# Performance work log

Measured on AMD Instinct MI355X. Metric: run time of the kernel, lower is better.

The kernel has to match this reference:

```python
import jax, jax.numpy as jnp
import numpy as np

TEMPERATURE = 8.0  # sqrt(d_k) with d_k = 64
NEG_INF = -jnp.inf


def setup_inputs() -> dict:
    key = jax.random.key(0)
    kq, kk, kv = jax.random.split(key, 3)
    b, n, d = 16, 2048, 64
    q = jax.random.normal(kq, (b, n, d), dtype=jnp.float32)
    k = jax.random.normal(kk, (b, n, d), dtype=jnp.float32)
    v = jax.random.normal(kv, (b, n, d), dtype=jnp.float32)
    # causal mask: True where attention is disallowed (strict upper triangle)
    mask = jnp.broadcast_to(jnp.triu(jnp.ones((n, n), dtype=bool), k=1), (b, n, n))
    return {"q": q, "k": k, "v": v, "mask": mask}


def reference(q, k, v, mask):
    # attn = q @ k^T / temperature   [b, n, n]
    attn = jnp.einsum('bqd,bkd->bqk', q, k) / TEMPERATURE
    attn = jnp.where(mask, NEG_INF, attn)
    attn = jax.nn.softmax(attn, axis=2)
    # output = attn @ v   [b, n, d]
    output = jnp.einsum('bqk,bkd->bqd', attn, v)
    return (output, attn)
```

## Files before the change

### kernel.cpp

```cpp
#include <hip/hip_runtime.h>


constexpr int B = 16;
constexpr int N = 2048;
constexpr int D = 64;
constexpr float INV_TEMP = 0.125f;

typedef __attribute__((ext_vector_type(8))) short bf16x8;
typedef __attribute__((ext_vector_type(4))) float f32x4;

__device__ __forceinline__ short f2bf(float f) {
    __bf16 h = (__bf16)f;
    return __builtin_bit_cast(short, h);
}

__global__ __launch_bounds__(256) void sdpa_mfma(
    const float* __restrict__ q,
    const float* __restrict__ k,
    const float* __restrict__ v,
    float* __restrict__ out,
    float* __restrict__ attn)
{
    const int x = blockIdx.x;
    const int b = x >> 5;
    const int u = x & 31;
    const int qt = (u & 1) ? (31 - (u >> 1)) : (u >> 1);
    const int qs = qt * 64;

    const int t    = threadIdx.x;
    const int w    = t >> 6;
    const int lane = t & 63;
    const int l15  = lane & 15;
    const int quad = lane >> 4;
    const int q8   = quad * 8;

    __shared__ __align__(16) short sK[64][72];
    __shared__ __align__(16) short sV[64][72];
    __shared__ __align__(16) short sP[4][16][72];

    const float* qb = q + (size_t)b * N * D;
    const float* kb = k + (size_t)b * N * D;
    const float* vb = v + (size_t)b * N * D;
    float* attn_b = attn + (size_t)b * N * N;

    const int srow = t >> 2;
    const int sd   = (t & 3) * 16;

    {
        const int ce = (qt + 1) * 64;
        float4 z = {0.f, 0.f, 0.f, 0.f};
        float* arow = attn_b + (size_t)(qs + srow) * N;
        for (int c = ce + (t & 3) * 16; c < N; c += 64) {
            float4* p4 = (float4*)(arow + c);
            p4[0] = z; p4[1] = z; p4[2] = z; p4[3] = z;
        }
    }

    {
        const float4* src = (const float4*)(qb + (size_t)(qs + srow) * D + sd);
        float4 f0 = src[0], f1 = src[1], f2 = src[2], f3 = src[3];
        float vals[16] = {f0.x,f0.y,f0.z,f0.w, f1.x,f1.y,f1.z,f1.w,
                          f2.x,f2.y,f2.z,f2.w, f3.x,f3.y,f3.z,f3.w};
        short* dst = &sK[srow][sd];
#pragma unroll
        for (int i = 0; i < 16; ++i) dst[i] = f2bf(vals[i]);
    }
    __syncthreads();
    const bf16x8 qa0 = *(const bf16x8*)&sK[w * 16 + l15][q8];
    const bf16x8 qa1 = *(const bf16x8*)&sK[w * 16 + l15][32 + q8];

    float rs[4] = {0.f, 0.f, 0.f, 0.f};
    for (int kt = 0; kt <= qt; ++kt) {
        __syncthreads();
        {
            const float4* src = (const float4*)(kb + (size_t)(kt * 64 + srow) * D + sd);
            float4 f0 = src[0], f1 = src[1], f2 = src[2], f3 = src[3];
            float vals[16] = {f0.x,f0.y,f0.z,f0.w, f1.x,f1.y,f1.z,f1.w,
                              f2.x,f2.y,f2.z,f2.w, f3.x,f3.y,f3.z,f3.w};
            short* dst = &sK[srow][sd];
#pragma unroll
            for (int i = 0; i < 16; ++i) dst[i] = f2bf(vals[i]);
        }
        __syncthreads();
        const bool diag = (kt == qt);
#pragma unroll
        for (int nt = 0; nt < 4; ++nt) {
            bf16x8 b0 = *(const bf16x8*)&sK[nt * 16 + l15][q8];
            bf16x8 b1 = *(const bf16x8*)&sK[nt * 16 + l15][32 + q8];
            f32x4 c = {0.f, 0.f, 0.f, 0.f};
            c = __builtin_amdgcn_mfma_f32_16x16x32_bf16(qa0, b0, c, 0, 0, 0);
            c = __builtin_amdgcn_mfma_f32_16x16x32_bf16(qa1, b1, c, 0, 0, 0);
            const int col = nt * 16 + l15;
#pragma unroll
            for (int r = 0; r < 4; ++r) {
                const int rowl = w * 16 + quad * 4 + r;
                float p = (!diag || col <= rowl) ? __expf(c[r] * INV_TEMP) : 0.f;
                rs[r] += p;
            }
        }
    }

    float inv[4];
#pragma unroll
    for (int r = 0; r < 4; ++r) {
        float s = rs[r];
        s += __shfl_xor(s, 1);
        s += __shfl_xor(s, 2);
        s += __shfl_xor(s, 4);
        s += __shfl_xor(s, 8);
        inv[r] = 1.f / s;
    }

    f32x4 o[4];
#pragma unroll
    for (int nt = 0; nt < 4; ++nt) o[nt] = {0.f, 0.f, 0.f, 0.f};

    for (int kt = 0; kt <= qt; ++kt) {
        __syncthreads();
        {
            const float4* src = (const float4*)(kb + (size_t)(kt * 64 + srow) * D + sd);
            float4 f0 = src[0], f1 = src[1], f2 = src[2], f3 = src[3];
            float vals[16] = {f0.x,f0.y,f0.z,f0.w, f1.x,f1.y,f1.z,f1.w,
                              f2.x,f2.y,f2.z,f2.w, f3.x,f3.y,f3.z,f3.w};
            short* dst = &sK[srow][sd];
#pragma unroll
            for (int i = 0; i < 16; ++i) dst[i] = f2bf(vals[i]);
        }
        {
            const float4* src = (const float4*)(vb + (size_t)(kt * 64 + srow) * D + sd);
            float4 f0 = src[0], f1 = src[1], f2 = src[2], f3 = src[3];
            float vals[16] = {f0.x,f0.y,f0.z,f0.w, f1.x,f1.y,f1.z,f1.w,
                              f2.x,f2.y,f2.z,f2.w, f3.x,f3.y,f3.z,f3.w};
#pragma unroll
            for (int i = 0; i < 16; ++i) sV[sd + i][srow] = f2bf(vals[i]);
        }
        __syncthreads();
        const bool diag = (kt == qt);
#pragma unroll
        for (int nt = 0; nt < 4; ++nt) {
            bf16x8 b0 = *(const bf16x8*)&sK[nt * 16 + l15][q8];
            bf16x8 b1 = *(const bf16x8*)&sK[nt * 16 + l15][32 + q8];
            f32x4 c = {0.f, 0.f, 0.f, 0.f};
            c = __builtin_amdgcn_mfma_f32_16x16x32_bf16(qa0, b0, c, 0, 0, 0);
            c = __builtin_amdgcn_mfma_f32_16x16x32_bf16(qa1, b1, c, 0, 0, 0);
            const int col = nt * 16 + l15;
            float* arow = attn_b + (size_t)(qs + w * 16 + quad * 4) * N + kt * 64 + col;
#pragma unroll
            for (int r = 0; r < 4; ++r) {
                const int rowl = w * 16 + quad * 4 + r;
                float p = (!diag || col <= rowl) ? __expf(c[r] * INV_TEMP) * inv[r] : 0.f;
                arow[(size_t)r * N] = p;
                sP[w][quad * 4 + r][col] = f2bf(p);
            }
        }
#pragma unroll
        for (int kc = 0; kc < 2; ++kc) {
            bf16x8 a = *(const bf16x8*)&sP[w][l15][kc * 32 + q8];
#pragma unroll
            for (int nt = 0; nt < 4; ++nt) {
                bf16x8 vf = *(const bf16x8*)&sV[nt * 16 + l15][kc * 32 + q8];
                o[nt] = __builtin_amdgcn_mfma_f32_16x16x32_bf16(a, vf, o[nt], 0, 0, 0);
            }
        }
    }

#pragma unroll
    for (int nt = 0; nt < 4; ++nt) {
        float* orow = out + (size_t)(b * N + qs + w * 16 + quad * 4) * D + nt * 16 + l15;
#pragma unroll
        for (int r = 0; r < 4; ++r) orow[(size_t)r * D] = o[nt][r];
    }
}

extern "C" void kernel_launch(void* const* d_in, const int* in_sizes, int n_in,
                              void* d_out, int out_size, void* d_ws, size_t ws_size,
                              hipStream_t stream) {
    const float* q = (const float*)d_in[0];
    const float* k = (const float*)d_in[1];
    const float* v = (const float*)d_in[2];

    float* out  = (float*)d_out;
    float* attn = out + (size_t)B * N * D;

    sdpa_mfma<<<dim3(B * 32), dim3(256), 0, stream>>>(q, k, v, out, attn);
}
```

Baseline: 514.4 us.

## Pre-convert Q/K/V to bf16 in workspace and read MFMA operands directly from global

```diff
diff --git a/kernel.cpp b/kernel.cpp
--- a/kernel.cpp
+++ b/kernel.cpp
@@ -5,6 +5,7 @@
 constexpr int N = 2048;
 constexpr int D = 64;
 constexpr float INV_TEMP = 0.125f;
+constexpr size_t QK_ELEMS = (size_t)B * N * D;
 
 typedef __attribute__((ext_vector_type(8))) short bf16x8;
 typedef __attribute__((ext_vector_type(4))) float f32x4;
@@ -14,12 +15,50 @@
     return __builtin_bit_cast(short, h);
 }
 
-__global__ __launch_bounds__(256) void sdpa_mfma(
-    const float* __restrict__ q,
-    const float* __restrict__ k,
-    const float* __restrict__ v,
-    float* __restrict__ out,
-    float* __restrict__ attn)
+__global__ __launch_bounds__(256) void sdpa_convert(
+    const float* __restrict__ q, const float* __restrict__ k, const float* __restrict__ v,
+    short* __restrict__ qbf, short* __restrict__ kbf, short* __restrict__ vt)
+{
+    const int blk = blockIdx.x;
+    const int t = threadIdx.x;
+    if (blk < 512) {
+        __shared__ short sT[64][72];
+        const int b = blk >> 5, n0 = (blk & 31) * 64;
+        const int srow = t >> 2, sd = (t & 3) * 16;
+        const float4* src = (const float4*)(v + ((size_t)b * N + n0 + srow) * D + sd);
+        float4 f0 = src[0], f1 = src[1], f2 = src[2], f3 = src[3];
+        float vals[16] = {f0.x,f0.y,f0.z,f0.w, f1.x,f1.y,f1.z,f1.w,
+                          f2.x,f2.y,f2.z,f2.w, f3.x,f3.y,f3.z,f3.w};
+        short* dst = &sT[srow][sd];
+#pragma unroll
+        for (int i = 0; i < 16; ++i) dst[i] = f2bf(vals[i]);
+        __syncthreads();
+        const int d = t >> 2, nc = (t & 3) * 16;
+        bf16x8 o0, o1;
+#pragma unroll
+        for (int i = 0; i < 8; ++i) o0[i] = sT[nc + i][d];
+#pragma unroll
+        for (int i = 0; i < 8; ++i) o1[i] = sT[nc + 8 + i][d];
+        short* dstv = vt + ((size_t)b * D + d) * N + n0 + nc;
+        *(bf16x8*)dstv = o0;
+        *(bf16x8*)(dstv + 8) = o1;
+    } else {
+        size_t gi = (size_t)(blk - 512) * 2048 + (size_t)t * 8;
+        const float* src; short* dst;
+        if (gi < QK_ELEMS) { src = q + gi;             dst = qbf + gi; }
+        else               { src = k + (gi - QK_ELEMS); dst = kbf + (gi - QK_ELEMS); }
+        float4 f0 = ((const float4*)src)[0];
+        float4 f1 = ((const float4*)src)[1];
+        bf16x8 o;
+        o[0]=f2bf(f0.x); o[1]=f2bf(f0.y); o[2]=f2bf(f0.z); o[3]=f2bf(f0.w);
+        o[4]=f2bf(f1.x); o[5]=f2bf(f1.y); o[6]=f2bf(f1.z); o[7]=f2bf(f1.w);
+        *(bf16x8*)dst = o;
+    }
+}
+
+__global__ __launch_bounds__(256) void sdpa_main(
+    const short* __restrict__ qbf, const short* __restrict__ kbf, const short* __restrict__ vt,
+    float* __restrict__ out, float* __restrict__ attn)
 {
     const int x = blockIdx.x;
     const int b = x >> 5;
@@ -34,19 +73,14 @@
     const int quad = lane >> 4;
     const int q8   = quad * 8;
 
-    __shared__ __align__(16) short sK[64][72];
-    __shared__ __align__(16) short sV[64][72];
     __shared__ __align__(16) short sP[4][16][72];
 
-    const float* qb = q + (size_t)b * N * D;
-    const float* kb = k + (size_t)b * N * D;
-    const float* vb = v + (size_t)b * N * D;
+    const short* kb  = kbf + (size_t)b * N * D;
+    const short* vtb = vt  + (size_t)b * D * N;
     float* attn_b = attn + (size_t)b * N * N;
 
-    const int srow = t >> 2;
-    const int sd   = (t & 3) * 16;
-
     {
+        const int srow = t >> 2;
         const int ce = (qt + 1) * 64;
         float4 z = {0.f, 0.f, 0.f, 0.f};
         float* arow = attn_b + (size_t)(qs + srow) * N;
@@ -56,37 +90,18 @@
         }
     }
 
-    {
-        const float4* src = (const float4*)(qb + (size_t)(qs + srow) * D + sd);
-        float4 f0 = src[0], f1 = src[1], f2 = src[2], f3 = src[3];
-        float vals[16] = {f0.x,f0.y,f0.z,f0.w, f1.x,f1.y,f1.z,f1.w,
-                          f2.x,f2.y,f2.z,f2.w, f3.x,f3.y,f3.z,f3.w};
-        short* dst = &sK[srow][sd];
-#pragma unroll
-        for (int i = 0; i < 16; ++i) dst[i] = f2bf(vals[i]);
-    }
-    __syncthreads();
-    const bf16x8 qa0 = *(const bf16x8*)&sK[w * 16 + l15][q8];
-    const bf16x8 qa1 = *(const bf16x8*)&sK[w * 16 + l15][32 + q8];
+    const short* qrow = qbf + ((size_t)b * N + qs + w * 16 + l15) * D;
+    const bf16x8 qa0 = *(const bf16x8*)(qrow + q8);
+    const bf16x8 qa1 = *(const bf16x8*)(qrow + 32 + q8);
 
     float rs[4] = {0.f, 0.f, 0.f, 0.f};
     for (int kt = 0; kt <= qt; ++kt) {
-        __syncthreads();
-        {
-            const float4* src = (const float4*)(kb + (size_t)(kt * 64 + srow) * D + sd);
-            float4 f0 = src[0], f1 = src[1], f2 = src[2], f3 = src[3];
-            float vals[16] = {f0.x,f0.y,f0.z,f0.w, f1.x,f1.y,f1.z,f1.w,
-                              f2.x,f2.y,f2.z,f2.w, f3.x,f3.y,f3.z,f3.w};
-            short* dst = &sK[srow][sd];
-#pragma unroll
-            for (int i = 0; i < 16; ++i) dst[i] = f2bf(vals[i]);
-        }
-        __syncthreads();
         const bool diag = (kt == qt);
 #pragma unroll
         for (int nt = 0; nt < 4; ++nt) {
-            bf16x8 b0 = *(const bf16x8*)&sK[nt * 16 + l15][q8];
-            bf16x8 b1 = *(const bf16x8*)&sK[nt * 16 + l15][32 + q8];
+            const short* krow = kb + (size_t)(kt * 64 + nt * 16 + l15) * D;
+            bf16x8 b0 = *(const bf16x8*)(krow + q8);
+            bf16x8 b1 = *(const bf16x8*)(krow + 32 + q8);
             f32x4 c = {0.f, 0.f, 0.f, 0.f};
             c = __builtin_amdgcn_mfma_f32_16x16x32_bf16(qa0, b0, c, 0, 0, 0);
             c = __builtin_amdgcn_mfma_f32_16x16x32_bf16(qa1, b1, c, 0, 0, 0);
@@ -94,12 +109,10 @@
 #pragma unroll
             for (int r = 0; r < 4; ++r) {
                 const int rowl = w * 16 + quad * 4 + r;
-                float p = (!diag || col <= rowl) ? __expf(c[r] * INV_TEMP) : 0.f;
-                rs[r] += p;
+                rs[r] += (!diag || col <= rowl) ? __expf(c[r] * INV_TEMP) : 0.f;
             }
         }
     }
-
     float inv[4];
 #pragma unroll
     for (int r = 0; r < 4; ++r) {
@@ -113,33 +126,15 @@
 
     f32x4 o[4];
 #pragma unroll
-    for (int nt = 0; nt < 4; ++nt) o[nt] = {0.f, 0.f, 0.f, 0.f};
+    for (int nt = 0; nt < 4; ++nt) o[nt] = (f32x4){0.f, 0.f, 0.f, 0.f};
 
     for (int kt = 0; kt <= qt; ++kt) {
-        __syncthreads();
-        {
-            const float4* src = (const float4*)(kb + (size_t)(kt * 64 + srow) * D + sd);
-            float4 f0 = src[0], f1 = src[1], f2 = src[2], f3 = src[3];
-            float vals[16] = {f0.x,f0.y,f0.z,f0.w, f1.x,f1.y,f1.z,f1.w,
-                              f2.x,f2.y,f2.z,f2.w, f3.x,f3.y,f3.z,f3.w};
-            short* dst = &sK[srow][sd];
-#pragma unroll
-            for (int i = 0; i < 16; ++i) dst[i] = f2bf(vals[i]);
-        }
-        {
-            const float4* src = (const float4*)(vb + (size_t)(kt * 64 + srow) * D + sd);
-            float4 f0 = src[0], f1 = src[1], f2 = src[2], f3 = src[3];
-            float vals[16] = {f0.x,f0.y,f0.z,f0.w, f1.x,f1.y,f1.z,f1.w,
-                              f2.x,f2.y,f2.z,f2.w, f3.x,f3.y,f3.z,f3.w};
-#pragma unroll
-            for (int i = 0; i < 16; ++i) sV[sd + i][srow] = f2bf(vals[i]);
-        }
-        __syncthreads();
         const bool diag = (kt == qt);
 #pragma unroll
         for (int nt = 0; nt < 4; ++nt) {
-            bf16x8 b0 = *(const bf16x8*)&sK[nt * 16 + l15][q8];
-            bf16x8 b1 = *(const bf16x8*)&sK[nt * 16 + l15][32 + q8];
+            const short* krow = kb + (size_t)(kt * 64 + nt * 16 + l15) * D;
+            bf16x8 b0 = *(const bf16x8*)(krow + q8);
+            bf16x8 b1 = *(const bf16x8*)(krow + 32 + q8);
             f32x4 c = {0.f, 0.f, 0.f, 0.f};
             c = __builtin_amdgcn_mfma_f32_16x16x32_bf16(qa0, b0, c, 0, 0, 0);
             c = __builtin_amdgcn_mfma_f32_16x16x32_bf16(qa1, b1, c, 0, 0, 0);
@@ -158,7 +153,8 @@
             bf16x8 a = *(const bf16x8*)&sP[w][l15][kc * 32 + q8];
 #pragma unroll
             for (int nt = 0; nt < 4; ++nt) {
-                bf16x8 vf = *(const bf16x8*)&sV[nt * 16 + l15][kc * 32 + q8];
+                const short* vrow = vtb + (size_t)(nt * 16 + l15) * N + kt * 64 + kc * 32 + q8;
+                bf16x8 vf = *(const bf16x8*)vrow;
                 o[nt] = __builtin_amdgcn_mfma_f32_16x16x32_bf16(a, vf, o[nt], 0, 0, 0);
             }
         }
@@ -166,7 +162,7 @@
 
 #pragma unroll
     for (int nt = 0; nt < 4; ++nt) {
-        float* orow = out + (size_t)(b * N + qs + w * 16 + quad * 4) * D + nt * 16 + l15;
+        float* orow = out + ((size_t)(b * N + qs + w * 16 + quad * 4)) * D + nt * 16 + l15;
 #pragma unroll
         for (int r = 0; r < 4; ++r) orow[(size_t)r * D] = o[nt][r];
     }
@@ -182,5 +178,10 @@
     float* out  = (float*)d_out;
     float* attn = out + (size_t)B * N * D;
 
-    sdpa_mfma<<<dim3(B * 32), dim3(256), 0, stream>>>(q, k, v, out, attn);
+    short* qbf = (short*)d_ws;
+    short* kbf = qbf + QK_ELEMS;
+    short* vtb = kbf + QK_ELEMS;
+
+    sdpa_convert<<<dim3(2560), dim3(256), 0, stream>>>(q, k, v, qbf, kbf, vtb);
+    sdpa_main<<<dim3(B * 32), dim3(256), 0, stream>>>(qbf, kbf, vtb, out, attn);
 }
```

Result: slower. 551.2 us (+7.1%).
